# Kernel tuning notes

Hardware: AMD Instinct MI355X
Metric: run time of the kernel (lower is better)

The kernel has to match this reference:

```python
import jax, jax.numpy as jnp
import numpy as np

B, T, E, H = 4, 2048, 1024, 16
HS = E // H
FF = 4 * E


def _layernorm(x, g, b, eps=1e-5):
    mu = jnp.mean(x, axis=-1, keepdims=True)
    var = jnp.var(x, axis=-1, keepdims=True)
    return (x - mu) * jax.lax.rsqrt(var + eps) * g + b


def setup_inputs() -> dict:
    key = jax.random.key(0)
    ks = jax.random.split(key, 12)
    s = E ** -0.5
    return {
        "x": jax.random.normal(ks[0], (B, T, E), jnp.float32),
        "Wq": jax.random.normal(ks[1], (E, E), jnp.float32) * s,
        "Wk": jax.random.normal(ks[2], (E, E), jnp.float32) * s,
        "Wv": jax.random.normal(ks[3], (E, E), jnp.float32) * s,
        "Wp": jax.random.normal(ks[4], (E, E), jnp.float32) * s,
        "bp": jnp.zeros((E,), jnp.float32),
        "W1": jax.random.normal(ks[5], (E, FF), jnp.float32) * s,
        "b1": jnp.zeros((FF,), jnp.float32),
        "W2": jax.random.normal(ks[6], (FF, E), jnp.float32) * (FF ** -0.5),
        "b2": jnp.zeros((E,), jnp.float32),
        "g1": jnp.ones((E,), jnp.float32),
        "be1": jnp.zeros((E,), jnp.float32),
        "g2": jnp.ones((E,), jnp.float32),
        "be2": jnp.zeros((E,), jnp.float32),
    }


def reference(x, Wq, Wk, Wv, Wp, bp, W1, b1, W2, b2, g1, be1, g2, be2):
    h = _layernorm(x, g1, be1)
    # per-head projections: Wq columns laid out head-by-head (matches concat order)
    q = (h @ Wq).reshape(B, T, H, HS).transpose(0, 2, 1, 3)  # [B,H,T,hs]
    k = (h @ Wk).reshape(B, T, H, HS).transpose(0, 2, 1, 3)
    v = (h @ Wv).reshape(B, T, H, HS).transpose(0, 2, 1, 3)
    # NOTE: original scales by full embedding size C**-0.5, not head_size
    scores = jnp.einsum("bhqd,bhkd->bhqk", q, k) * (E ** -0.5)
    causal = jnp.tril(jnp.ones((T, T), bool))
    scores = jnp.where(causal, scores, -jnp.inf)
    wei = jax.nn.softmax(scores, axis=-1)
    attn = jnp.einsum("bhqk,bhkd->bhqd", wei, v)  # [B,H,T,hs]
    attn = attn.transpose(0, 2, 1, 3).reshape(B, T, E)
    x = x + attn @ Wp + bp
    h2 = _layernorm(x, g2, be2)
    ff = jax.nn.relu(h2 @ W1 + b1) @ W2 + b2
    return x + ff
```

## Files before the change

### kernel.cpp

```cpp
#include <hip/hip_runtime.h>
#include <stdint.h>

typedef unsigned short u16;
typedef short s8v __attribute__((ext_vector_type(8)));
typedef float f32x4 __attribute__((ext_vector_type(4)));

#define B_SZ 4
#define T_SEQ 2048
#define E_DIM 1024
#define H_NUM 16
#define HS 64
#define FF_DIM 4096
#define M_ROWS 8192
#define QSCALE 0.0450842200f

__device__ __forceinline__ u16 f2bf(float f) {
    unsigned int u = __builtin_bit_cast(unsigned int, f);
    u += 0x7fffu + ((u >> 16) & 1u);
    return (u16)(u >> 16);
}

__device__ __forceinline__ float bf2f(u16 u) {
    unsigned int v = ((unsigned int)u) << 16;
    return __builtin_bit_cast(float, v);
}

__device__ __forceinline__ void async_copy16(const void* g, void* l) {
    __builtin_amdgcn_global_load_lds(
        (const __attribute__((address_space(1))) unsigned int*)g,
        (__attribute__((address_space(3))) unsigned int*)l, 16, 0, 0);
}

__global__ __launch_bounds__(256)
void transpose_cast4(const float* __restrict__ s0, const float* __restrict__ s1,
                     const float* __restrict__ s2, const float* __restrict__ s3,
                     u16* __restrict__ dqkv, u16* __restrict__ dp) {
    __shared__ float tile[32][33];
    const int zz = blockIdx.z;
    const float* src = (zz == 0) ? s0 : (zz == 1) ? s1 : (zz == 2) ? s2 : s3;
    u16* dst = (zz < 3) ? dqkv + (size_t)zz * 1048576 : dp;
    int n0 = blockIdx.x * 32, k0 = blockIdx.y * 32;
    int tx = threadIdx.x, ty = threadIdx.y;
#pragma unroll
    for (int i = 0; i < 4; i++)
        tile[ty + i * 8][tx] = src[(size_t)(k0 + ty + i * 8) * 1024 + n0 + tx];
    __syncthreads();
#pragma unroll
    for (int i = 0; i < 4; i++)
        dst[(size_t)(n0 + ty + i * 8) * 1024 + k0 + tx] = f2bf(tile[tx][ty + i * 8]);
}

__global__ __launch_bounds__(256)
void transpose_cast_w12(const float* __restrict__ W1, const float* __restrict__ W2,
                        u16* __restrict__ d1, u16* __restrict__ d2) {
    __shared__ float tile[32][33];
    const int zz = blockIdx.z;
    const float* src;
    u16* dst;
    int n0, k0, N, K;
    if (zz == 0) {
        src = W1; dst = d1; N = 4096; K = 1024;
        n0 = blockIdx.x * 32; k0 = blockIdx.y * 32;
    } else {
        src = W2; dst = d2; N = 1024; K = 4096;
        int idx = blockIdx.y * 128 + blockIdx.x;
        n0 = (idx & 31) * 32; k0 = (idx >> 5) * 32;
    }
    int tx = threadIdx.x, ty = threadIdx.y;
#pragma unroll
    for (int i = 0; i < 4; i++)
        tile[ty + i * 8][tx] = src[(size_t)(k0 + ty + i * 8) * N + n0 + tx];
    __syncthreads();
#pragma unroll
    for (int i = 0; i < 4; i++)
        dst[(size_t)(n0 + ty + i * 8) * K + k0 + tx] = f2bf(tile[tx][ty + i * 8]);
}

__global__ __launch_bounds__(256)
void transpose_v(const u16* __restrict__ V, u16* __restrict__ VT) {
    __shared__ u16 tile[64][80];
    const int t0 = blockIdx.x * 64;
    const size_t hoff = (size_t)blockIdx.y * (T_SEQ * HS);
    const int r = threadIdx.x >> 2, c0 = (threadIdx.x & 3) * 16;
    const u16* src = V + hoff + (size_t)(t0 + r) * HS + c0;
    *(s8v*)&tile[r][c0] = *(const s8v*)src;
    *(s8v*)&tile[r][c0 + 8] = *(const s8v*)(src + 8);
    __syncthreads();
    u16 tmp[16];
#pragma unroll
    for (int e = 0; e < 16; e++) tmp[e] = tile[c0 + e][r];
    u16* dst = VT + hoff + (size_t)r * T_SEQ + t0 + c0;
    *(s8v*)dst = *(const s8v*)&tmp[0];
    *(s8v*)(dst + 8) = *(const s8v*)&tmp[8];
}

__global__ __launch_bounds__(256)
void ln_kernel(const float* __restrict__ x, const float* __restrict__ g,
               const float* __restrict__ b, u16* __restrict__ out) {
    int row = blockIdx.x;
    int tid = threadIdx.x;
    float4 v = ((const float4*)(x + (size_t)row * E_DIM))[tid];
    float s = v.x + v.y + v.z + v.w;
    float sq = v.x * v.x + v.y * v.y + v.z * v.z + v.w * v.w;
#pragma unroll
    for (int off = 32; off; off >>= 1) {
        s += __shfl_xor(s, off);
        sq += __shfl_xor(sq, off);
    }
    __shared__ float sh[8];
    int w = tid >> 6, lane = tid & 63;
    if (lane == 0) { sh[w] = s; sh[4 + w] = sq; }
    __syncthreads();
    s = sh[0] + sh[1] + sh[2] + sh[3];
    sq = sh[4] + sh[5] + sh[6] + sh[7];
    float mu = s * (1.f / E_DIM);
    float var = sq * (1.f / E_DIM) - mu * mu;
    float rs = rsqrtf(var + 1e-5f);
    float4 gv = ((const float4*)g)[tid];
    float4 bv = ((const float4*)b)[tid];
    ushort4 o;
    o.x = f2bf((v.x - mu) * rs * gv.x + bv.x);
    o.y = f2bf((v.y - mu) * rs * gv.y + bv.y);
    o.z = f2bf((v.z - mu) * rs * gv.z + bv.z);
    o.w = f2bf((v.w - mu) * rs * gv.w + bv.w);
    ((ushort4*)(out + (size_t)row * E_DIM))[tid] = o;
}

__global__ __launch_bounds__(256)
void ln_kernel_bf(const u16* __restrict__ x, const float* __restrict__ g,
                  const float* __restrict__ b, u16* __restrict__ out) {
    int row = blockIdx.x;
    int tid = threadIdx.x;
    ushort4 uv = ((const ushort4*)(x + (size_t)row * E_DIM))[tid];
    float4 v;
    v.x = bf2f(uv.x); v.y = bf2f(uv.y); v.z = bf2f(uv.z); v.w = bf2f(uv.w);
    float s = v.x + v.y + v.z + v.w;
    float sq = v.x * v.x + v.y * v.y + v.z * v.z + v.w * v.w;
#pragma unroll
    for (int off = 32; off; off >>= 1) {
        s += __shfl_xor(s, off);
        sq += __shfl_xor(sq, off);
    }
    __shared__ float sh[8];
    int w = tid >> 6, lane = tid & 63;
    if (lane == 0) { sh[w] = s; sh[4 + w] = sq; }
    __syncthreads();
    s = sh[0] + sh[1] + sh[2] + sh[3];
    sq = sh[4] + sh[5] + sh[6] + sh[7];
    float mu = s * (1.f / E_DIM);
    float var = sq * (1.f / E_DIM) - mu * mu;
    float rs = rsqrtf(var + 1e-5f);
    float4 gv = ((const float4*)g)[tid];
    float4 bv = ((const float4*)b)[tid];
    ushort4 o;
    o.x = f2bf((v.x - mu) * rs * gv.x + bv.x);
    o.y = f2bf((v.y - mu) * rs * gv.y + bv.y);
    o.z = f2bf((v.z - mu) * rs * gv.z + bv.z);
    o.w = f2bf((v.w - mu) * rs * gv.w + bv.w);
    ((ushort4*)(out + (size_t)row * E_DIM))[tid] = o;
}

template <int MODE>
__global__ __launch_bounds__(512)
void gemm_bt128(const u16* __restrict__ A, const u16* __restrict__ BT,
                int M, int N, int K,
                const float* __restrict__ bias, const float* __restrict__ resid,
                float* __restrict__ outf, u16* __restrict__ outb) {
    __shared__ __align__(16) u16 As[3][256 * 64];
    __shared__ __align__(16) u16 Bs[3][128 * 64];

    const int gx = gridDim.x;
    const int nwg = gx * gridDim.y;
    const int l = blockIdx.y * gx + blockIdx.x;
    const int sw = (l & 7) * (nwg >> 3) + (l >> 3);
    const int tRow = (sw / gx) * 256, tCol = (sw % gx) * 128;

    const int tid = threadIdx.x, w = tid >> 6, lane = tid & 63;
    const int wr = w >> 1, wc = w & 1, lr = lane & 15, hg = lane >> 4;
    const int nk = K >> 6;

    f32x4 z = {0.f, 0.f, 0.f, 0.f};
    f32x4 acc[4][4];
#pragma unroll
    for (int m = 0; m < 4; m++)
#pragma unroll
        for (int n = 0; n < 4; n++) acc[m][n] = z;

    auto STAGE_A = [&](int kt, int c) {
#pragma unroll
        for (int i = 0; i < 4; i++) {
            int chunk = i * 512 + tid;
            int row = chunk >> 3, j = chunk & 7;
            int js = (j ^ (row & 7)) << 3;
            async_copy16(A + (size_t)(tRow + row) * K + (kt << 6) + js,
                         &As[c][(i * 512 + w * 64) * 8]);
        }
    };
    auto STAGE_B = [&](int kt, int c) {
#pragma unroll
        for (int i = 0; i < 2; i++) {
            int chunk = i * 512 + tid;
            int row = chunk >> 3, j = chunk & 7;
            int js = (j ^ (row & 7)) << 3;
            async_copy16(BT + (size_t)(tCol + row) * K + (kt << 6) + js,
                         &Bs[c][(i * 512 + w * 64) * 8]);
        }
    };

    STAGE_A(0, 0); STAGE_B(0, 0);
    STAGE_A(1, 1); STAGE_B(1, 1);
    asm volatile("s_waitcnt vmcnt(6)" ::: "memory");
    asm volatile("s_barrier" ::: "memory");

    for (int t = 0; t < nk; ++t) {
        const int bu = t % 3, nx = (t + 2) % 3;
        const u16* Ab = &As[bu][0];
        const u16* Bb = &Bs[bu][0];
        const bool more = (t + 2 < nk);

        s8v af0[2][2], bf[4][2];
#pragma unroll
        for (int m = 0; m < 2; m++)
#pragma unroll
            for (int kk = 0; kk < 2; kk++) {
                int r = wr * 64 + m * 16 + lr;
                af0[m][kk] = *(const s8v*)&Ab[r * 64 + (((kk * 4 + hg) ^ (r & 7)) << 3)];
            }
#pragma unroll
        for (int n = 0; n < 4; n++)
#pragma unroll
            for (int kk = 0; kk < 2; kk++) {
                int r = wc * 64 + n * 16 + lr;
                bf[n][kk] = *(const s8v*)&Bb[r * 64 + (((kk * 4 + hg) ^ (r & 7)) << 3)];
            }
        if (more) STAGE_A(t + 2, nx);
        asm volatile("s_barrier" ::: "memory");
        __builtin_amdgcn_s_setprio(1);
#pragma unroll
        for (int m = 0; m < 2; m++)
#pragma unroll
            for (int n = 0; n < 4; n++)
#pragma unroll
                for (int kk = 0; kk < 2; kk++)
                    acc[m][n] = __builtin_amdgcn_mfma_f32_16x16x32_bf16(
                        af0[m][kk], bf[n][kk], acc[m][n], 0, 0, 0);
        __builtin_amdgcn_s_setprio(0);
        asm volatile("s_barrier" ::: "memory");

        s8v af1[2][2];
#pragma unroll
        for (int m = 0; m < 2; m++)
#pragma unroll
            for (int kk = 0; kk < 2; kk++) {
                int r = wr * 64 + (m + 2) * 16 + lr;
                af1[m][kk] = *(const s8v*)&Ab[r * 64 + (((kk * 4 + hg) ^ (r & 7)) << 3)];
            }
        if (more) STAGE_B(t + 2, nx);
        asm volatile("s_barrier" ::: "memory");
        __builtin_amdgcn_s_setprio(1);
#pragma unroll
        for (int m = 0; m < 2; m++)
#pragma unroll
            for (int n = 0; n < 4; n++)
#pragma unroll
                for (int kk = 0; kk < 2; kk++)
                    acc[m + 2][n] = __builtin_amdgcn_mfma_f32_16x16x32_bf16(
                        af1[m][kk], bf[n][kk], acc[m + 2][n], 0, 0, 0);
        __builtin_amdgcn_s_setprio(0);
        if (more) asm volatile("s_waitcnt vmcnt(6)" ::: "memory");
        else      asm volatile("s_waitcnt vmcnt(0)" ::: "memory");
        asm volatile("s_barrier" ::: "memory");
    }

#pragma unroll
    for (int m = 0; m < 4; m++)
#pragma unroll
        for (int n = 0; n < 4; n++)
#pragma unroll
            for (int r = 0; r < 4; r++) {
                int row = tRow + wr * 64 + m * 16 + hg * 4 + r;
                int col = tCol + wc * 64 + n * 16 + lr;
                float v = acc[m][n][r];
                if (MODE == 0) {
                    int type = col >> 10, c2 = col & 1023;
                    int h = c2 >> 6, d = c2 & 63;
                    int bb = row >> 11, tt = row & 2047;
                    if (type == 0) v *= QSCALE;
                    outb[(size_t)type * 8388608 +
                         (((size_t)(bb * H_NUM + h) * T_SEQ + tt) << 6) + d] = f2bf(v);
                } else if (MODE == 1) {
                    v += bias[col];
                    v = fmaxf(v, 0.f);
                    outb[(size_t)row * N + col] = f2bf(v);
                } else {
                    outb[(size_t)row * N + col] =
                        f2bf(resid[(size_t)row * N + col] + v + bias[col]);
                }
            }
}

template <int MODE>
__global__ __launch_bounds__(512)
void gemm_bt256(const u16* __restrict__ A, const u16* __restrict__ BT,
                int M, int N, int Kst, int klen,
                const float* __restrict__ bias, const float* __restrict__ resid,
                float* __restrict__ outf, u16* __restrict__ outb) {
    __shared__ __align__(16) u16 As[2][256 * 64];
    __shared__ __align__(16) u16 Bs[2][256 * 64];

    const int gx = gridDim.x;
    const int nwg = gx * gridDim.y;
    const int l = blockIdx.y * gx + blockIdx.x;
    const int sw = (l & 7) * (nwg >> 3) + (l >> 3);
    const int tRow = (sw / gx) * 256, tCol = (sw % gx) * 256;
    const size_t koff = (size_t)blockIdx.z * klen;
    const u16* Az = A + koff;
    const u16* BTz = BT + koff;

    const int tid = threadIdx.x, w = tid >> 6, lane = tid & 63;
    const int wr = w >> 2, wc = w & 3, lr = lane & 15, hg = lane >> 4;
    const int nk = klen >> 6;

    f32x4 z = {0.f, 0.f, 0.f, 0.f};
    f32x4 acc[8][4];
#pragma unroll
    for (int m = 0; m < 8; m++)
#pragma unroll
        for (int n = 0; n < 4; n++) acc[m][n] = z;

    auto STAGE_A = [&](int kt, int c, int h) {
#pragma unroll
        for (int i = 0; i < 2; i++) {
            int chunk = h * 1024 + i * 512 + tid;
            int row = chunk >> 3, j = chunk & 7;
            int js = (j ^ (row & 7)) << 3;
            async_copy16(Az + (size_t)(tRow + row) * Kst + (kt << 6) + js,
                         &As[c][(h * 1024 + i * 512 + w * 64) * 8]);
        }
    };
    auto STAGE_B = [&](int kt, int c, int h) {
#pragma unroll
        for (int i = 0; i < 2; i++) {
            int chunk = h * 1024 + i * 512 + tid;
            int row = chunk >> 3, j = chunk & 7;
            int js = (j ^ (row & 7)) << 3;
            async_copy16(BTz + (size_t)(tCol + row) * Kst + (kt << 6) + js,
                         &Bs[c][(h * 1024 + i * 512 + w * 64) * 8]);
        }
    };

    STAGE_B(0, 0, 0); STAGE_B(0, 0, 1); STAGE_A(0, 0, 0); STAGE_A(0, 0, 1);
    STAGE_B(1, 1, 0); STAGE_B(1, 1, 1); STAGE_A(1, 1, 0); STAGE_A(1, 1, 1);
    asm volatile("s_waitcnt vmcnt(6)" ::: "memory");
    asm volatile("s_barrier" ::: "memory");

    for (int t = 0; t < nk; ++t) {
        const int cur = t & 1;
        const u16* Ab = &As[cur][0];
        const u16* Bb = &Bs[cur][0];
        const bool more = (t + 2 < nk);

        s8v bf[4][2];
#pragma unroll
        for (int p = 0; p < 4; p++) {
            s8v af[2][2];
#pragma unroll
            for (int mm = 0; mm < 2; mm++)
#pragma unroll
                for (int kk = 0; kk < 2; kk++) {
                    int r = (2 * p + mm) * 32 + wr * 16 + lr;
                    af[mm][kk] = *(const s8v*)&Ab[r * 64 + (((kk * 4 + hg) ^ (r & 7)) << 3)];
                }
            if (p == 0) {
#pragma unroll
                for (int n = 0; n < 4; n++)
#pragma unroll
                    for (int kk = 0; kk < 2; kk++) {
                        int r = n * 64 + wc * 16 + lr;
                        bf[n][kk] = *(const s8v*)&Bb[r * 64 + (((kk * 4 + hg) ^ (r & 7)) << 3)];
                    }
            }
            if (more) {
                if (p == 0) STAGE_B(t + 2, cur, 0);
                else if (p == 1) STAGE_B(t + 2, cur, 1);
                else if (p == 2) STAGE_A(t + 2, cur, 0);
                else STAGE_A(t + 2, cur, 1);
            }
            asm volatile("s_barrier" ::: "memory");
            __builtin_amdgcn_s_setprio(1);
#pragma unroll
            for (int mm = 0; mm < 2; mm++)
#pragma unroll
                for (int n = 0; n < 4; n++)
#pragma unroll
                    for (int kk = 0; kk < 2; kk++)
                        acc[2 * p + mm][n] = __builtin_amdgcn_mfma_f32_16x16x32_bf16(
                            af[mm][kk], bf[n][kk], acc[2 * p + mm][n], 0, 0, 0);
            __builtin_amdgcn_s_setprio(0);
            if (p == 3) {
                if (more) asm volatile("s_waitcnt vmcnt(6)" ::: "memory");
                else      asm volatile("s_waitcnt vmcnt(0)" ::: "memory");
            }
            asm volatile("s_barrier" ::: "memory");
        }
    }

    u16* outp = outb;
    if (MODE == 3 && blockIdx.z == 1) outp = (u16*)outf;
#pragma unroll
    for (int m = 0; m < 8; m++)
#pragma unroll
        for (int n = 0; n < 4; n++)
#pragma unroll
            for (int r = 0; r < 4; r++) {
                int row = tRow + m * 32 + wr * 16 + hg * 4 + r;
                int col = tCol + n * 64 + wc * 16 + lr;
                float v = acc[m][n][r];
                if (MODE == 1) {
                    v += bias[col];
                    v = fmaxf(v, 0.f);
                    outp[(size_t)row * N + col] = f2bf(v);
                } else {
                    outp[(size_t)row * N + col] = f2bf(v);
                }
            }
}

__global__ __launch_bounds__(256)
void reduce_w2(const u16* __restrict__ p0, const u16* __restrict__ p1,
               const u16* __restrict__ resid, const float* __restrict__ bias,
               float* __restrict__ out) {
    const int total = M_ROWS * E_DIM / 4;
    for (int i = blockIdx.x * 256 + threadIdx.x; i < total; i += gridDim.x * 256) {
        ushort4 rr = ((const ushort4*)resid)[i];
        float4 bb = ((const float4*)bias)[i & 255];
        ushort4 a = ((const ushort4*)p0)[i];
        ushort4 c = ((const ushort4*)p1)[i];
        float4 o;
        o.x = bf2f(a.x) + bf2f(c.x) + bf2f(rr.x) + bb.x;
        o.y = bf2f(a.y) + bf2f(c.y) + bf2f(rr.y) + bb.y;
        o.z = bf2f(a.z) + bf2f(c.z) + bf2f(rr.z) + bb.z;
        o.w = bf2f(a.w) + bf2f(c.w) + bf2f(rr.w) + bb.w;
        ((float4*)out)[i] = o;
    }
}

__global__ __launch_bounds__(512)
void attn_kernel(const u16* __restrict__ Q, const u16* __restrict__ K,
                 const u16* __restrict__ VT, u16* __restrict__ O) {
    __shared__ u16 Ks[2][64 * 64];
    __shared__ u16 Vs[2][64 * 64];
    __shared__ u16 Pl[8][16 * 64];
    const int bh = blockIdx.y;
    const u16* Qh = Q + (size_t)bh * T_SEQ * HS;
    const u16* Kh = K + (size_t)bh * T_SEQ * HS;
    const u16* VTh = VT + (size_t)bh * T_SEQ * HS;
    const int tid = threadIdx.x, w = tid >> 6, lane = tid & 63;
    const int lr = lane & 15, hg = lane >> 4;
    const int swz = (lr & 7) << 3;
    const int bb = bh >> 4, hh = bh & 15;
    const f32x4 z = {0.f, 0.f, 0.f, 0.f};

    for (int half = 0; half < 2; ++half) {
        const int qt = half ? (15 - blockIdx.x) : blockIdx.x;
        const int qb = qt * 128;
        const int nt = 2 * qt + 2;

        s8v qf[2];
        {
            const int qrow = qb + w * 16 + lr;
            qf[0] = *(const s8v*)(Qh + (size_t)qrow * HS + hg * 8);
            qf[1] = *(const s8v*)(Qh + (size_t)qrow * HS + 32 + hg * 8);
        }
        f32x4 o[4] = {z, z, z, z};
        float m_run[4] = {0.f, 0.f, 0.f, 0.f};
        float l_part[4] = {0.f, 0.f, 0.f, 0.f};

        auto STAGE = [&](int t, int c) {
            int chunk = tid;
            int row = chunk >> 3, j = chunk & 7;
            int js = (j ^ (row & 7)) << 3;
            async_copy16(Kh + (size_t)t * (64 * HS) + row * HS + js, &Ks[c][w * 512]);
            async_copy16(VTh + (size_t)row * T_SEQ + t * 64 + js, &Vs[c][w * 512]);
        };

        int cur = 0;
        STAGE(0, 0);
        __syncthreads();

        for (int t = 0; t < nt; ++t) {
            if (t + 1 < nt) STAGE(t + 1, cur ^ 1);

            f32x4 s[4];
            __builtin_amdgcn_s_setprio(1);
#pragma unroll
            for (int n = 0; n < 4; n++) {
                f32x4 a = z;
#pragma unroll
                for (int kc = 0; kc < 2; kc++) {
                    s8v bfr = *(const s8v*)&Ks[cur][((n * 16 + lr) * 64 + kc * 32 + hg * 8) ^ swz];
                    a = __builtin_amdgcn_mfma_f32_16x16x32_bf16(qf[kc], bfr, a, 0, 0, 0);
                }
                s[n] = a;
            }
            __builtin_amdgcn_s_setprio(0);
            const bool diag = (t >= nt - 2);
            if (diag) {
#pragma unroll
                for (int n = 0; n < 4; n++)
#pragma unroll
                    for (int r = 0; r < 4; r++)
                        if ((t * 64 + n * 16 + lr) > (qb + w * 16 + hg * 4 + r))
                            s[n][r] = -1e30f;
            }
            float d0[4][4], p4[4][4];
#pragma unroll
            for (int n = 0; n < 4; n++)
#pragma unroll
                for (int r = 0; r < 4; r++) {
                    d0[n][r] = s[n][r] - m_run[r];
                    p4[n][r] = __builtin_amdgcn_exp2f(d0[n][r]);
                }
            float sm[4];
#pragma unroll
            for (int r = 0; r < 4; r++)
                sm[r] = (p4[0][r] + p4[1][r]) + (p4[2][r] + p4[3][r]);
            float smax = fmaxf(fmaxf(sm[0], sm[1]), fmaxf(sm[2], sm[3]));
            if (__any(!(smax <= 2048.f))) {
                float pm[4];
#pragma unroll
                for (int r = 0; r < 4; r++) {
                    float m0 = fmaxf(fmaxf(d0[0][r], d0[1][r]), fmaxf(d0[2][r], d0[3][r]));
                    m0 = fmaxf(m0, __shfl_xor(m0, 1));
                    m0 = fmaxf(m0, __shfl_xor(m0, 2));
                    m0 = fmaxf(m0, __shfl_xor(m0, 4));
                    m0 = fmaxf(m0, __shfl_xor(m0, 8));
                    pm[r] = fmaxf(m0, 0.f);
                }
#pragma unroll
                for (int r = 0; r < 4; r++) {
                    float al = __builtin_amdgcn_exp2f(-pm[r]);
                    m_run[r] += pm[r];
                    l_part[r] *= al;
                    o[0][r] *= al; o[1][r] *= al; o[2][r] *= al; o[3][r] *= al;
                }
#pragma unroll
                for (int n = 0; n < 4; n++)
#pragma unroll
                    for (int r = 0; r < 4; r++)
                        p4[n][r] = __builtin_amdgcn_exp2f(d0[n][r] - pm[r]);
#pragma unroll
                for (int r = 0; r < 4; r++)
                    sm[r] = (p4[0][r] + p4[1][r]) + (p4[2][r] + p4[3][r]);
            }
#pragma unroll
            for (int r = 0; r < 4; r++) l_part[r] += sm[r];
            u16* Pw = &Pl[w][0];
#pragma unroll
            for (int n = 0; n < 4; n++)
#pragma unroll
                for (int r = 0; r < 4; r++) {
                    int prow = hg * 4 + r;
                    Pw[(prow * 64 + n * 16 + lr) ^ ((prow & 7) << 3)] =
                        (u16)(__builtin_bit_cast(unsigned int, p4[n][r]) >> 16);
                }
            asm volatile("s_waitcnt lgkmcnt(0)" ::: "memory");
            __builtin_amdgcn_s_setprio(1);
#pragma unroll
            for (int n = 0; n < 4; n++) {
#pragma unroll
                for (int kc = 0; kc < 2; kc++) {
                    s8v pa = *(const s8v*)&Pw[(lr * 64 + kc * 32 + hg * 8) ^ swz];
                    s8v vb = *(const s8v*)&Vs[cur][((n * 16 + lr) * 64 + kc * 32 + hg * 8) ^ swz];
                    o[n] = __builtin_amdgcn_mfma_f32_16x16x32_bf16(pa, vb, o[n], 0, 0, 0);
                }
            }
            __builtin_amdgcn_s_setprio(0);
            __syncthreads();
            cur ^= 1;
        }
        float rl[4];
#pragma unroll
        for (int r = 0; r < 4; r++) {
            float lsum = l_part[r];
            lsum += __shfl_xor(lsum, 1);
            lsum += __shfl_xor(lsum, 2);
            lsum += __shfl_xor(lsum, 4);
            lsum += __shfl_xor(lsum, 8);
            rl[r] = 1.f / lsum;
        }
#pragma unroll
        for (int n = 0; n < 4; n++)
#pragma unroll
            for (int r = 0; r < 4; r++) {
                int trow = qb + w * 16 + hg * 4 + r;
                O[((size_t)(bb * T_SEQ + trow)) * E_DIM + hh * HS + n * 16 + lr] =
                    f2bf(o[n][r] * rl[r]);
            }
    }
}

extern "C" void kernel_launch(void* const* d_in, const int* in_sizes, int n_in,
                              void* d_out, int out_size, void* d_ws, size_t ws_size,
                              hipStream_t stream) {
    (void)in_sizes; (void)n_in; (void)out_size; (void)ws_size;
    const float* x  = (const float*)d_in[0];
    const float* Wq = (const float*)d_in[1];
    const float* Wk = (const float*)d_in[2];
    const float* Wv = (const float*)d_in[3];
    const float* Wp = (const float*)d_in[4];
    const float* bp = (const float*)d_in[5];
    const float* W1 = (const float*)d_in[6];
    const float* b1 = (const float*)d_in[7];
    const float* W2 = (const float*)d_in[8];
    const float* b2 = (const float*)d_in[9];
    const float* g1  = (const float*)d_in[10];
    const float* be1 = (const float*)d_in[11];
    const float* g2  = (const float*)d_in[12];
    const float* be2 = (const float*)d_in[13];

    char* ws = (char*)d_ws;
    u16* wqkv_t  = (u16*)(ws);
    u16* wp_t    = (u16*)(ws + 6291456);
    u16* w1_t    = (u16*)(ws + 8388608);
    u16* w2_t    = (u16*)(ws + 16777216);
    u16* h_bf    = (u16*)(ws + 25165824);
    u16* q_bf    = (u16*)(ws + 41943040);
    u16* attn_bf = q_bf + 3 * 8388608;
    u16* ff1     = q_bf;
    u16* x2b     = (u16*)(ws + 109051904);
    u16* vt_bf   = h_bf;
    u16* part0   = (u16*)ws;
    u16* part1   = h_bf;

    dim3 b32(32, 8);
    transpose_cast4<<<dim3(32, 32, 4), b32, 0, stream>>>(Wq, Wk, Wv, Wp, wqkv_t, wp_t);
    transpose_cast_w12<<<dim3(128, 32, 2), b32, 0, stream>>>(W1, W2, w1_t, w2_t);

    ln_kernel<<<M_ROWS, 256, 0, stream>>>(x, g1, be1, h_bf);
    gemm_bt128<0><<<dim3(24, 32), 512, 0, stream>>>(h_bf, wqkv_t, M_ROWS, 3072, 1024,
                                                    nullptr, nullptr, nullptr, q_bf);
    transpose_v<<<dim3(32, 64), 256, 0, stream>>>(q_bf + 2 * 8388608, vt_bf);
    attn_kernel<<<dim3(8, 64), 512, 0, stream>>>(q_bf, q_bf + 8388608, vt_bf, attn_bf);
    gemm_bt128<2><<<dim3(8, 32), 512, 0, stream>>>(attn_bf, wp_t, M_ROWS, 1024, 1024,
                                                   bp, x, nullptr, x2b);
    ln_kernel_bf<<<M_ROWS, 256, 0, stream>>>(x2b, g2, be2, h_bf);
    gemm_bt256<1><<<dim3(16, 32), 512, 0, stream>>>(h_bf, w1_t, M_ROWS, 4096, 1024, 1024,
                                                    b1, nullptr, nullptr, ff1);
    gemm_bt256<3><<<dim3(4, 32, 2), 512, 0, stream>>>(ff1, w2_t, M_ROWS, 1024, 4096, 2048,
                                                      nullptr, nullptr, (float*)part1, part0);
    reduce_w2<<<2048, 256, 0, stream>>>(part0, part1, x2b, b2, (float*)d_out);
}
```

Before: 343.7 us.

## Fuse V transpose into QKV GEMM epilogue and drop split-K W2 reduction

The QKV GEMM epilogue now writes V directly in transposed [b,h,d,t] layout with packed 4-element stores, which removes the separate transpose_v kernel. The W2 GEMM switches from a split-K 256x256 kernel plus a reduce kernel to the 128-wide GEMM with a new mode. That mode adds the bias and bf16 residual and writes fp32 output in its epilogue. This removes two launches and the partial-sum round trip. In exchange the W2 GEMM loses split-K parallelism (256 workgroups with full K=4096) and uses a different tile shape.

Measured after the change: 338.9 us. Within noise of the previous version (-1.4%).

```diff
diff --git a/kernel.cpp b/kernel.cpp
--- a/kernel.cpp
+++ b/kernel.cpp
@@ -74,24 +74,6 @@
 #pragma unroll
     for (int i = 0; i < 4; i++)
         dst[(size_t)(n0 + ty + i * 8) * K + k0 + tx] = f2bf(tile[tx][ty + i * 8]);
-}
-
-__global__ __launch_bounds__(256)
-void transpose_v(const u16* __restrict__ V, u16* __restrict__ VT) {
-    __shared__ u16 tile[64][80];
-    const int t0 = blockIdx.x * 64;
-    const size_t hoff = (size_t)blockIdx.y * (T_SEQ * HS);
-    const int r = threadIdx.x >> 2, c0 = (threadIdx.x & 3) * 16;
-    const u16* src = V + hoff + (size_t)(t0 + r) * HS + c0;
-    *(s8v*)&tile[r][c0] = *(const s8v*)src;
-    *(s8v*)&tile[r][c0 + 8] = *(const s8v*)(src + 8);
-    __syncthreads();
-    u16 tmp[16];
-#pragma unroll
-    for (int e = 0; e < 16; e++) tmp[e] = tile[c0 + e][r];
-    u16* dst = VT + hoff + (size_t)r * T_SEQ + t0 + c0;
-    *(s8v*)dst = *(const s8v*)&tmp[0];
-    *(s8v*)(dst + 8) = *(const s8v*)&tmp[8];
 }
 
 __global__ __launch_bounds__(256)
@@ -164,7 +146,7 @@
 __global__ __launch_bounds__(512)
 void gemm_bt128(const u16* __restrict__ A, const u16* __restrict__ BT,
                 int M, int N, int K,
-                const float* __restrict__ bias, const float* __restrict__ resid,
+                const float* __restrict__ bias, const void* __restrict__ residv,
                 float* __restrict__ outf, u16* __restrict__ outb) {
     __shared__ __align__(16) u16 As[3][256 * 64];
     __shared__ __align__(16) u16 Bs[3][128 * 64];
@@ -275,28 +257,52 @@
 #pragma unroll
     for (int m = 0; m < 4; m++)
 #pragma unroll
-        for (int n = 0; n < 4; n++)
-#pragma unroll
-            for (int r = 0; r < 4; r++) {
-                int row = tRow + wr * 64 + m * 16 + hg * 4 + r;
+        for (int n = 0; n < 4; n++) {
+            if (MODE == 0) {
                 int col = tCol + wc * 64 + n * 16 + lr;
-                float v = acc[m][n][r];
-                if (MODE == 0) {
-                    int type = col >> 10, c2 = col & 1023;
-                    int h = c2 >> 6, d = c2 & 63;
-                    int bb = row >> 11, tt = row & 2047;
-                    if (type == 0) v *= QSCALE;
-                    outb[(size_t)type * 8388608 +
-                         (((size_t)(bb * H_NUM + h) * T_SEQ + tt) << 6) + d] = f2bf(v);
-                } else if (MODE == 1) {
-                    v += bias[col];
-                    v = fmaxf(v, 0.f);
-                    outb[(size_t)row * N + col] = f2bf(v);
+                int type = col >> 10, c2 = col & 1023;
+                int h = c2 >> 6, d = c2 & 63;
+                int row0 = tRow + wr * 64 + m * 16 + hg * 4;
+                int bb = row0 >> 11, t0 = row0 & 2047;
+                if (type == 2) {
+                    ushort4 pk;
+                    pk.x = f2bf(acc[m][n][0]);
+                    pk.y = f2bf(acc[m][n][1]);
+                    pk.z = f2bf(acc[m][n][2]);
+                    pk.w = f2bf(acc[m][n][3]);
+                    u16* vt = (u16*)outf;
+                    *(ushort4*)&vt[(((size_t)(bb * H_NUM + h) * 64 + d) << 11) + t0] = pk;
                 } else {
-                    outb[(size_t)row * N + col] =
-                        f2bf(resid[(size_t)row * N + col] + v + bias[col]);
-                }
-            }
+#pragma unroll
+                    for (int r = 0; r < 4; r++) {
+                        float v = acc[m][n][r];
+                        if (type == 0) v *= QSCALE;
+                        outb[(size_t)type * 8388608 +
+                             (((size_t)(bb * H_NUM + h) * T_SEQ + t0 + r) << 6) + d] = f2bf(v);
+                    }
+                }
+            } else {
+#pragma unroll
+                for (int r = 0; r < 4; r++) {
+                    int row = tRow + wr * 64 + m * 16 + hg * 4 + r;
+                    int col = tCol + wc * 64 + n * 16 + lr;
+                    float v = acc[m][n][r];
+                    if (MODE == 1) {
+                        v += bias[col];
+                        v = fmaxf(v, 0.f);
+                        outb[(size_t)row * N + col] = f2bf(v);
+                    } else if (MODE == 2) {
+                        const float* resid = (const float*)residv;
+                        outb[(size_t)row * N + col] =
+                            f2bf(resid[(size_t)row * N + col] + v + bias[col]);
+                    } else {
+                        const u16* resid = (const u16*)residv;
+                        outf[(size_t)row * N + col] =
+                            bf2f(resid[(size_t)row * N + col]) + v + bias[col];
+                    }
+                }
+            }
+        }
 }
 
 template <int MODE>
@@ -405,8 +411,6 @@
         }
     }
 
-    u16* outp = outb;
-    if (MODE == 3 && blockIdx.z == 1) outp = (u16*)outf;
 #pragma unroll
     for (int m = 0; m < 8; m++)
 #pragma unroll
@@ -416,33 +420,10 @@
                 int row = tRow + m * 32 + wr * 16 + hg * 4 + r;
                 int col = tCol + n * 64 + wc * 16 + lr;
                 float v = acc[m][n][r];
-                if (MODE == 1) {
-                    v += bias[col];
-                    v = fmaxf(v, 0.f);
-                    outp[(size_t)row * N + col] = f2bf(v);
-                } else {
-                    outp[(size_t)row * N + col] = f2bf(v);
-                }
-            }
-}
-
-__global__ __launch_bounds__(256)
-void reduce_w2(const u16* __restrict__ p0, const u16* __restrict__ p1,
-               const u16* __restrict__ resid, const float* __restrict__ bias,
-               float* __restrict__ out) {
-    const int total = M_ROWS * E_DIM / 4;
-    for (int i = blockIdx.x * 256 + threadIdx.x; i < total; i += gridDim.x * 256) {
-        ushort4 rr = ((const ushort4*)resid)[i];
-        float4 bb = ((const float4*)bias)[i & 255];
-        ushort4 a = ((const ushort4*)p0)[i];
-        ushort4 c = ((const ushort4*)p1)[i];
-        float4 o;
-        o.x = bf2f(a.x) + bf2f(c.x) + bf2f(rr.x) + bb.x;
-        o.y = bf2f(a.y) + bf2f(c.y) + bf2f(rr.y) + bb.y;
-        o.z = bf2f(a.z) + bf2f(c.z) + bf2f(rr.z) + bb.z;
-        o.w = bf2f(a.w) + bf2f(c.w) + bf2f(rr.w) + bb.w;
-        ((float4*)out)[i] = o;
-    }
+                v += bias[col];
+                v = fmaxf(v, 0.f);
+                outb[(size_t)row * N + col] = f2bf(v);
+            }
 }
 
 __global__ __launch_bounds__(512)
@@ -626,12 +607,10 @@
     u16* w2_t    = (u16*)(ws + 16777216);
     u16* h_bf    = (u16*)(ws + 25165824);
     u16* q_bf    = (u16*)(ws + 41943040);
+    u16* vt_bf   = q_bf + 2 * 8388608;
     u16* attn_bf = q_bf + 3 * 8388608;
     u16* ff1     = q_bf;
     u16* x2b     = (u16*)(ws + 109051904);
-    u16* vt_bf   = h_bf;
-    u16* part0   = (u16*)ws;
-    u16* part1   = h_bf;
 
     dim3 b32(32, 8);
     transpose_cast4<<<dim3(32, 32, 4), b32, 0, stream>>>(Wq, Wk, Wv, Wp, wqkv_t, wp_t);
@@ -639,15 +618,13 @@
 
     ln_kernel<<<M_ROWS, 256, 0, stream>>>(x, g1, be1, h_bf);
     gemm_bt128<0><<<dim3(24, 32), 512, 0, stream>>>(h_bf, wqkv_t, M_ROWS, 3072, 1024,
-                                                    nullptr, nullptr, nullptr, q_bf);
-    transpose_v<<<dim3(32, 64), 256, 0, stream>>>(q_bf + 2 * 8388608, vt_bf);
+                                                    nullptr, nullptr, (float*)vt_bf, q_bf);
     attn_kernel<<<dim3(8, 64), 512, 0, stream>>>(q_bf, q_bf + 8388608, vt_bf, attn_bf);
     gemm_bt128<2><<<dim3(8, 32), 512, 0, stream>>>(attn_bf, wp_t, M_ROWS, 1024, 1024,
                                                    bp, x, nullptr, x2b);
     ln_kernel_bf<<<M_ROWS, 256, 0, stream>>>(x2b, g2, be2, h_bf);
     gemm_bt256<1><<<dim3(16, 32), 512, 0, stream>>>(h_bf, w1_t, M_ROWS, 4096, 1024, 1024,
                                                     b1, nullptr, nullptr, ff1);
-    gemm_bt256<3><<<dim3(4, 32, 2), 512, 0, stream>>>(ff1, w2_t, M_ROWS, 1024, 4096, 2048,
-                                                      nullptr, nullptr, (float*)part1, part0);
-    reduce_w2<<<2048, 256, 0, stream>>>(part0, part1, x2b, b2, (float*)d_out);
-}
+    gemm_bt128<4><<<dim3(8, 32), 512, 0, stream>>>(ff1, w2_t, M_ROWS, 1024, 4096,
+                                                   b2, x2b, (float*)d_out, nullptr);
+}
```
